# Performance work log

Hardware: AMD Instinct MI355X
Metric: run time of the kernel (lower is better)

Reference implementation:

```python
import jax, jax.numpy as jnp
import numpy as np

B, T, C = 16, 512, 1024
D, K, W = 4096, 128, 8


def _scatter_topk(a, k, use_values):
    """Top-k along last axis; return dense array with top-k values (or 1.0) scattered, zeros elsewhere."""
    shp = a.shape
    a2 = a.reshape(-1, shp[-1])
    vals, idx = jax.lax.top_k(a2, k)
    rows = jnp.arange(a2.shape[0])[:, None]
    src = vals if use_values else jnp.ones_like(vals)
    return jnp.zeros_like(a2).at[rows, idx].set(src).reshape(shp)


def _window_topk(x, k, window_size):
    # x: (B, T, D)
    b, t, d = x.shape
    stride = max(1, window_size // 2)
    if stride >= t:
        num_windows, pad, t_pad = 1, 0, t
    else:
        num_windows = (t - window_size) // stride + 1
        required = (num_windows - 1) * stride + window_size
        pad = max(0, required - t)
        t_pad = t + pad
    if pad > 0:
        x = jnp.pad(x, ((0, 0), (0, pad), (0, 0)))
    starts = jnp.arange(num_windows) * stride                      # (NW,)
    tidx = starts[:, None] + jnp.arange(window_size)               # (NW, W)
    x_windows = x[:, tidx, :]                                      # (B, NW, W, D)
    window_sums = x_windows.sum(axis=2)                            # (B, NW, D)
    mask_windows = _scatter_topk(window_sums, k, use_values=False)  # (B, NW, D)
    votes = (x_windows * mask_windows[:, :, None, :]).reshape(b, num_windows * window_size, d)
    feature_votes = jnp.zeros((b, t_pad, d), x.dtype).at[:, tidx.reshape(-1)].add(votes)
    mask_combined = _scatter_topk(feature_votes, k, use_values=False)  # (B, Tp, D)
    x_sparse = x * mask_combined
    return x_sparse[:, :t - 0, :] if pad > 0 else x_sparse


def setup_inputs() -> dict:
    key = jax.random.key(0)
    ks = jax.random.split(key, 4)
    x_ssl = jax.random.normal(ks[0], (B, T, C), jnp.float32)
    W_dec = jax.random.normal(ks[1], (C, D), jnp.float32)
    W_dec = W_dec / jnp.linalg.norm(W_dec, axis=0, keepdims=True)
    W_enc = W_dec.T                                                # tied init, as in module
    W1 = jax.random.normal(ks[2], (256, D), jnp.float32) * (1.0 / np.sqrt(D))
    W2 = jax.random.normal(ks[3], (2, 256), jnp.float32) * (1.0 / np.sqrt(256))
    return dict(
        x_ssl=x_ssl, W_enc=W_enc, b_enc=jnp.zeros((D,), jnp.float32),
        W_dec=W_dec, b_dec=jnp.zeros((C,), jnp.float32),
        ln_g=jnp.ones((D,), jnp.float32), ln_b=jnp.zeros((D,), jnp.float32),
        W1=W1, b1=jnp.zeros((256,), jnp.float32),
        W2=W2, b2=jnp.zeros((2,), jnp.float32),
    )


def reference(x_ssl, W_enc, b_enc, W_dec, b_dec, ln_g, ln_b, W1, b1, W2, b2):
    b, t, c = x_ssl.shape
    x_flat = x_ssl.reshape(b * t, c)
    # SAE encode with window top-k (window_size=8 > 1 path)
    pre = jnp.einsum('nc,dc->nd', x_flat - b_dec, W_enc) + b_enc
    post_relu = jax.nn.relu(pre).reshape(b, t, -1)                 # (B, T, D)
    encoded = _window_topk(post_relu, K, W)                        # (B, T, D)
    encoded_flat = encoded.reshape(b * t, -1)
    # SAE decode + reconstruction loss
    x_recon = jnp.einsum('nd,cd->nc', encoded_flat, W_dec) + b_dec
    sae_loss = jnp.mean((x_recon - x_flat) ** 2)
    # classifier on pooled sparse features (dropout is inference no-op)
    pooled = encoded.mean(axis=1)                                  # (B, D) == AdaptiveAvgPool1d(1)
    mu = pooled.mean(axis=-1, keepdims=True)
    var = pooled.var(axis=-1, keepdims=True)
    ln = (pooled - mu) / jnp.sqrt(var + 1e-5) * ln_g + ln_b
    h = jax.nn.relu(ln @ W1.T + b1)
    logits = h @ W2.T + b2
    log_probs = jax.nn.log_softmax(logits, axis=-1)
    return log_probs, sae_loss
```

## Files before the change

### kernel.cpp

```cpp
#include <hip/hip_runtime.h>

#define BB   16
#define TT   512
#define CC   1024
#define DD   4096
#define NN   (BB*TT)
#define NWIN 127
#define KTOP 128

typedef __attribute__((ext_vector_type(8))) short short8;
typedef _Float16 half8 __attribute__((ext_vector_type(8)));
typedef __attribute__((ext_vector_type(4))) float f32x4;

__device__ __forceinline__ unsigned short f2bf(float f) {
    unsigned u = __float_as_uint(f);
    unsigned r = (u + 0x7fffu + ((u >> 16) & 1u)) >> 16;
    return (unsigned short)r;
}
__device__ __forceinline__ float bf2f(unsigned x) {
    return __uint_as_float((x & 0xffffu) << 16);
}
__device__ __forceinline__ unsigned short f2h(float f) {
    union { _Float16 h; unsigned short u; } c;
    c.h = (_Float16)f;
    return c.u;
}
__device__ __forceinline__ unsigned tokey(float f) {
    unsigned u = __float_as_uint(f);
    return (u & 0x80000000u) ? ~u : (u | 0x80000000u);
}
__device__ __forceinline__ void async_lds16(const void* g, void* l) {
    __builtin_amdgcn_global_load_lds((const __attribute__((address_space(1))) void*)g,
                                     (__attribute__((address_space(3))) void*)l, 16, 0, 0);
}

__device__ __forceinline__ unsigned wave_prefix_incl(unsigned v) {
    int lane = threadIdx.x & 63;
#pragma unroll
    for (int off = 1; off < 64; off <<= 1) {
        unsigned n = __shfl_up(v, off, 64);
        if (lane >= off) v += n;
    }
    return v;
}
__device__ __forceinline__ unsigned wave_suffix_incl(unsigned v) {
    int lane = threadIdx.x & 63;
#pragma unroll
    for (int off = 1; off < 64; off <<= 1) {
        unsigned n = __shfl_down(v, off, 64);
        if (lane + off < 64) v += n;
    }
    return v;
}

__device__ __forceinline__ unsigned select_top128(const unsigned* keys,
                                                  unsigned* hist, unsigned* shx) {
    const int tid = threadIdx.x, wid = tid >> 6, lane = tid & 63;
    const unsigned ZKEY = 0x80000000u;
    unsigned cpos = 0, cz = 0;
#pragma unroll
    for (int i = 0; i < 16; ++i) {
        cpos += (keys[i] > ZKEY);
        cz   += (keys[i] == ZKEY);
    }
    unsigned ppos = wave_prefix_incl(cpos);
    unsigned pz   = wave_prefix_incl(cz);
    if (lane == 63) { shx[wid] = ppos; shx[4 + wid] = pz; }
    __syncthreads();
    unsigned nz = shx[0] + shx[1] + shx[2] + shx[3];
    unsigned selbits = 0u;
    if (nz <= KTOP) {
        unsigned need = KTOP - nz;
        unsigned zr = pz - cz;
        if (wid > 0) zr += shx[4];
        if (wid > 1) zr += shx[5];
        if (wid > 2) zr += shx[6];
#pragma unroll
        for (int i = 0; i < 16; ++i) {
            bool sel = (keys[i] > ZKEY) || (keys[i] == ZKEY && zr < need);
            if (keys[i] == ZKEY) ++zr;
            selbits |= (sel ? 1u : 0u) << i;
        }
        return selbits;
    }
    unsigned k2[16];
#pragma unroll
    for (int i = 0; i < 16; ++i) k2[i] = (keys[i] > ZKEY) ? keys[i] : 0u;
    unsigned prefix = 0u, pmask = 0u, Kr = KTOP;
    for (int shift = 24; shift >= 0; shift -= 8) {
        hist[tid] = 0u; hist[256 + tid] = 0u; hist[512 + tid] = 0u; hist[768 + tid] = 0u;
        __syncthreads();
        unsigned* h = hist + (wid << 8);
#pragma unroll
        for (int i = 0; i < 16; ++i)
            if (k2[i] && (k2[i] & pmask) == prefix) atomicAdd(&h[(k2[i] >> shift) & 255u], 1u);
        __syncthreads();
        unsigned v = hist[tid] + hist[256 + tid] + hist[512 + tid] + hist[768 + tid];
        unsigned s = wave_suffix_incl(v);
        if (lane == 0) shx[wid] = s;
        __syncthreads();
        unsigned stot = s;
        if (wid == 0) stot += shx[1] + shx[2] + shx[3];
        else if (wid == 1) stot += shx[2] + shx[3];
        else if (wid == 2) stot += shx[3];
        unsigned above = stot - v;
        if (stot >= Kr && above < Kr) { shx[8] = (unsigned)tid; shx[9] = Kr - above; }
        __syncthreads();
        prefix |= shx[8] << shift;
        pmask |= 0xFFu << shift;
        Kr = shx[9];
    }
    unsigned T = prefix, need = Kr;
    unsigned ce = 0;
#pragma unroll
    for (int i = 0; i < 16; ++i) ce += (k2[i] == T);
    unsigned pe = wave_prefix_incl(ce);
    __syncthreads();
    if (lane == 63) shx[4 + wid] = pe;
    __syncthreads();
    unsigned er = pe - ce;
    if (wid > 0) er += shx[4];
    if (wid > 1) er += shx[5];
    if (wid > 2) er += shx[6];
#pragma unroll
    for (int i = 0; i < 16; ++i) {
        bool sel = (k2[i] > T) || (k2[i] == T && er < need);
        if (k2[i] == T) ++er;
        selbits |= (sel ? 1u : 0u) << i;
    }
    return selbits;
}

__global__ __launch_bounds__(256) void k_convert_all(const float* __restrict__ x,
                                                     const float* __restrict__ Wenc,
                                                     const float* __restrict__ Wdec,
                                                     const float* __restrict__ bdec,
                                                     unsigned short* __restrict__ xh,
                                                     unsigned short* __restrict__ wh,
                                                     unsigned short* __restrict__ wdb,
                                                     float* __restrict__ pooled_zero) {
    const int bid = blockIdx.x;
    if (bid < 8192) {
        size_t i = (size_t)bid * 256 + threadIdx.x;
        float4 v = ((const float4*)x)[i];
        size_t c = (i * 4) & (CC - 1);
        v.x -= bdec[c]; v.y -= bdec[c + 1]; v.z -= bdec[c + 2]; v.w -= bdec[c + 3];
        uint2 o;
        o.x = (unsigned)f2h(v.x) | ((unsigned)f2h(v.y) << 16);
        o.y = (unsigned)f2h(v.z) | ((unsigned)f2h(v.w) << 16);
        ((uint2*)xh)[i] = o;
    } else if (bid < 12288) {
        size_t i = (size_t)(bid - 8192) * 256 + threadIdx.x;
        float4 v = ((const float4*)Wenc)[i];
        uint2 o;
        o.x = (unsigned)f2h(v.x) | ((unsigned)f2h(v.y) << 16);
        o.y = (unsigned)f2h(v.z) | ((unsigned)f2h(v.w) << 16);
        ((uint2*)wh)[i] = o;
    } else if (bid < 16384) {
        size_t i = (size_t)(bid - 12288) * 256 + threadIdx.x;
        float4 v = ((const float4*)Wdec)[i];
        uint2 o;
        o.x = (unsigned)f2bf(v.x) | ((unsigned)f2bf(v.y) << 16);
        o.y = (unsigned)f2bf(v.z) | ((unsigned)f2bf(v.w) << 16);
        ((uint2*)wdb)[i] = o;
    } else {
        const int n4 = (BB * DD + 64) / 4;
        for (int i = threadIdx.x; i < n4; i += 256)
            ((float4*)pooled_zero)[i] = make_float4(0.f, 0.f, 0.f, 0.f);
    }
}

__device__ __forceinline__ void stage_tile_swz(const unsigned short* gbase, size_t ldk,
                                               unsigned short* lds, int wave, int lane) {
    const int sub = lane >> 3;
    const int cj  = (lane & 7) ^ sub;
#pragma unroll
    for (int i = 0; i < 4; ++i) {
        int n = wave * 4 + i;
        int r = n * 8 + sub;
        async_lds16(gbase + (size_t)r * ldk + cj * 8, lds + n * 512);
    }
}

__global__ __launch_bounds__(256) void k_gemm_enc_f16(const unsigned short* __restrict__ Ah,
                                                      const unsigned short* __restrict__ Bh,
                                                      const float* __restrict__ bias,
                                                      float* __restrict__ Cout,
                                                      float* __restrict__ gsum,
                                                      int Ndim, int Kdim) {
    __shared__ __align__(16) unsigned short smem[2 * 128 * 64];
    unsigned short* At = smem;
    unsigned short* Bt = smem + 128 * 64;
    float* cbuf = (float*)smem;
    const int tid = threadIdx.x, wave = tid >> 6, lane = tid & 63;
    const int bm = blockIdx.y * 128, bn = blockIdx.x * 128;
    const int wm = (wave >> 1) * 64, wn = (wave & 1) * 64;
    const int rA = lane & 15, q8 = (lane >> 4) * 8, rp7 = rA & 7;
    const int q = lane >> 4, qr = q * 4, cl = lane & 15;
    f32x4 acc[4][4] = {};
    for (int k0 = 0; k0 < Kdim; k0 += 64) {
        __syncthreads();
        stage_tile_swz(Ah + (size_t)bm * Kdim + k0, Kdim, At, wave, lane);
        stage_tile_swz(Bh + (size_t)bn * Kdim + k0, Kdim, Bt, wave, lane);
        __syncthreads();
#pragma unroll
        for (int kk = 0; kk < 64; kk += 32) {
            const int sc = ((((kk + q8) >> 3) ^ rp7) << 3);
            half8 a[4], b[4];
#pragma unroll
            for (int mt = 0; mt < 4; ++mt) a[mt] = *(const half8*)(At + (wm + mt * 16 + rA) * 64 + sc);
#pragma unroll
            for (int nt = 0; nt < 4; ++nt) b[nt] = *(const half8*)(Bt + (wn + nt * 16 + rA) * 64 + sc);
#pragma unroll
            for (int mt = 0; mt < 4; ++mt)
#pragma unroll
                for (int nt = 0; nt < 4; ++nt)
                    acc[mt][nt] = __builtin_amdgcn_mfma_f32_16x16x32_f16(a[mt], b[nt], acc[mt][nt], 0, 0, 0);
        }
    }
    float bv[4];
#pragma unroll
    for (int nt = 0; nt < 4; ++nt) bv[nt] = bias[bn + wn + nt * 16 + cl];
#pragma unroll
    for (int p = 0; p < 2; ++p) {
        __syncthreads();
        if ((wave >> 1) == p) {
#pragma unroll
            for (int nt = 0; nt < 4; ++nt) {
                int lc = wn + nt * 16 + cl;
                int pcb = (lc >> 2) ^ (q << 1);
#pragma unroll
                for (int mt = 0; mt < 4; ++mt) {
#pragma unroll
                    for (int r = 0; r < 4; ++r) {
                        int lr = mt * 16 + qr + r;
                        float v = acc[mt][nt][r] + bv[nt];
                        v = v > 0.f ? v : 0.f;
                        cbuf[lr * 128 + pcb * 4 + (lc & 3)] = v;
                    }
                }
            }
        }
        __syncthreads();
#pragma unroll
        for (int i = 0; i < 2; ++i) {
            int gidx = i * 256 + tid;
            int grow = gidx >> 5;
            int colg = gidx & 31;
            float4 s = make_float4(0.f, 0.f, 0.f, 0.f);
#pragma unroll
            for (int j = 0; j < 4; ++j) {
                int lr = grow * 4 + j;
                int pcr = colg ^ (((lr >> 2) & 3) << 1);
                float4 v = *(const float4*)&cbuf[lr * 128 + pcr * 4];
                s.x += v.x; s.y += v.y; s.z += v.z; s.w += v.w;
                *(float4*)&Cout[(size_t)(bm + p * 64 + lr) * Ndim + bn + colg * 4] = v;
            }
            if (gsum)
                *(float4*)&gsum[(size_t)((bm >> 2) + p * 16 + grow) * Ndim + bn + colg * 4] = s;
        }
    }
}

__global__ __launch_bounds__(256) void k_gemm_recon(const unsigned short* __restrict__ A,
                                                    size_t lda,
                                                    const unsigned short* __restrict__ Bm,
                                                    const float* __restrict__ bdec,
                                                    const float* __restrict__ X,
                                                    float* __restrict__ sae,
                                                    int Ndim, int Kdim) {
    __shared__ __align__(16) unsigned short At[2][128 * 64];
    __shared__ __align__(16) unsigned short Bt[2][128 * 64];
    __shared__ float red[256];
    const int tid = threadIdx.x, wave = tid >> 6, lane = tid & 63;
    const int bm = blockIdx.y * 128, bn = blockIdx.x * 128;
    const int wm = (wave >> 1) * 64, wn = (wave & 1) * 64;
    const int rA = lane & 15, q8 = (lane >> 4) * 8, rp7 = rA & 7;
    f32x4 acc[4][4] = {};
    stage_tile_swz(A + (size_t)bm * lda, lda, At[0], wave, lane);
    stage_tile_swz(Bm + (size_t)bn * Kdim, Kdim, Bt[0], wave, lane);
    __syncthreads();
    for (int k0 = 0; k0 < Kdim; k0 += 64) {
        const int cur = (k0 >> 6) & 1;
        if (k0 + 64 < Kdim) {
            stage_tile_swz(A + (size_t)bm * lda + k0 + 64, lda, At[cur ^ 1], wave, lane);
            stage_tile_swz(Bm + (size_t)bn * Kdim + k0 + 64, Kdim, Bt[cur ^ 1], wave, lane);
        }
#pragma unroll
        for (int kk = 0; kk < 64; kk += 32) {
            const int sc = ((((kk + q8) >> 3) ^ rp7) << 3);
            short8 a[4], b[4];
#pragma unroll
            for (int mt = 0; mt < 4; ++mt) a[mt] = *(const short8*)(At[cur] + (wm + mt * 16 + rA) * 64 + sc);
#pragma unroll
            for (int nt = 0; nt < 4; ++nt) b[nt] = *(const short8*)(Bt[cur] + (wn + nt * 16 + rA) * 64 + sc);
#pragma unroll
            for (int mt = 0; mt < 4; ++mt)
#pragma unroll
                for (int nt = 0; nt < 4; ++nt)
                    acc[mt][nt] = __builtin_amdgcn_mfma_f32_16x16x32_bf16(a[mt], b[nt], acc[mt][nt], 0, 0, 0);
        }
        __syncthreads();
    }
    const int cl = lane & 15, qr = (lane >> 4) * 4;
    float lsum = 0.f;
#pragma unroll
    for (int nt = 0; nt < 4; ++nt) {
        int col = bn + wn + nt * 16 + cl;
        float bv = bdec[col];
#pragma unroll
        for (int mt = 0; mt < 4; ++mt) {
            int row0 = bm + wm + mt * 16 + qr;
#pragma unroll
            for (int r = 0; r < 4; ++r) {
                float v = acc[mt][nt][r] + bv - X[(size_t)(row0 + r) * Ndim + col];
                lsum += v * v;
            }
        }
    }
    red[tid] = lsum;
    __syncthreads();
    for (int s = 128; s > 0; s >>= 1) { if (tid < s) red[tid] += red[tid + s]; __syncthreads(); }
    if (tid == 0) atomicAdd(sae, red[0]);
}

__global__ __launch_bounds__(256) void k_winsum_g(const float* __restrict__ gsum,
                                                  unsigned* __restrict__ wmask) {
    __shared__ unsigned hist[1024];
    __shared__ unsigned shx[16];
    __shared__ unsigned short halves[256];
    const int tid = threadIdx.x, w = blockIdx.x, b = blockIdx.y;
    const float* g0 = gsum + ((size_t)(b * 128 + w)) * DD + tid * 16;
    const float* g1 = g0 + DD;
    unsigned keys[16];
#pragma unroll
    for (int q = 0; q < 4; ++q) {
        float4 u = *(const float4*)(g0 + q * 4);
        float4 v = *(const float4*)(g1 + q * 4);
        keys[q * 4 + 0] = tokey(u.x + v.x);
        keys[q * 4 + 1] = tokey(u.y + v.y);
        keys[q * 4 + 2] = tokey(u.z + v.z);
        keys[q * 4 + 3] = tokey(u.w + v.w);
    }
    unsigned selbits = select_top128(keys, hist, shx);
    halves[tid] = (unsigned short)selbits;
    __syncthreads();
    if (tid < 128)
        wmask[(size_t)(b * NWIN + w) * 128 + tid] =
            (unsigned)halves[2 * tid] | ((unsigned)halves[2 * tid + 1] << 16);
}

__global__ __launch_bounds__(256) void k_winsum_p(const float* __restrict__ post,
                                                  unsigned* __restrict__ wmask) {
    __shared__ unsigned hist[1024];
    __shared__ unsigned shx[16];
    __shared__ unsigned short halves[256];
    const int tid = threadIdx.x, w = blockIdx.x, b = blockIdx.y;
    const float* base = post + (size_t)(b * TT + w * 4) * DD + tid * 16;
    float s[16] = {};
#pragma unroll
    for (int j = 0; j < 8; ++j) {
        const float* rp = base + (size_t)j * DD;
#pragma unroll
        for (int q = 0; q < 4; ++q) {
            float4 u = *(const float4*)(rp + q * 4);
            s[q * 4 + 0] += u.x; s[q * 4 + 1] += u.y; s[q * 4 + 2] += u.z; s[q * 4 + 3] += u.w;
        }
    }
    unsigned keys[16];
#pragma unroll
    for (int i = 0; i < 16; ++i) keys[i] = tokey(s[i]);
    unsigned selbits = select_top128(keys, hist, shx);
    halves[tid] = (unsigned short)selbits;
    __syncthreads();
    if (tid < 128)
        wmask[(size_t)(b * NWIN + w) * 128 + tid] =
            (unsigned)halves[2 * tid] | ((unsigned)halves[2 * tid + 1] << 16);
}

__global__ __launch_bounds__(256) void k_votes(float* __restrict__ post,
                                               const unsigned* __restrict__ wmask,
                                               float* __restrict__ pooled) {
    __shared__ unsigned long long cand[256];
    __shared__ unsigned char selbyte[DD];
    __shared__ unsigned shx[16];
    const int tid = threadIdx.x, wid = tid >> 6, lane = tid & 63;
    const int t = blockIdx.x, b = blockIdx.y;
    float* rp = post + (size_t)(b * TT + t) * DD;
    int w1 = t >> 2, w0 = w1 - 1;
    unsigned mw0 = 0u, mw1 = 0u;
    if (w0 >= 0)        mw0 = wmask[(size_t)(b * NWIN + w0) * 128 + (tid >> 1)];
    if (w1 <= NWIN - 1) mw1 = wmask[(size_t)(b * NWIN + w1) * 128 + (tid >> 1)];
    const int bbase = (tid & 1) * 16;
    const unsigned ZKEY = 0x80000000u;
    float vals[16];
    unsigned keys[16];
#pragma unroll
    for (int q = 0; q < 4; ++q) {
        float4 u = *(const float4*)(rp + tid * 16 + q * 4);
        vals[q * 4 + 0] = u.x; vals[q * 4 + 1] = u.y; vals[q * 4 + 2] = u.z; vals[q * 4 + 3] = u.w;
    }
#pragma unroll
    for (int i = 0; i < 16; ++i) {
        float cov = (float)(((mw0 >> (bbase + i)) & 1u) + ((mw1 >> (bbase + i)) & 1u));
        keys[i] = tokey(vals[i] * cov);
    }
    unsigned cpos = 0, cz = 0;
#pragma unroll
    for (int i = 0; i < 16; ++i) {
        cpos += (keys[i] > ZKEY);
        cz   += (keys[i] == ZKEY);
    }
    unsigned ppos = wave_prefix_incl(cpos);
    unsigned pz   = wave_prefix_incl(cz);
    if (lane == 63) { shx[wid] = ppos; shx[4 + wid] = pz; }
    __syncthreads();
    unsigned nz = shx[0] + shx[1] + shx[2] + shx[3];
    unsigned selbits = 0u;
    if (nz <= KTOP) {
        unsigned need = KTOP - nz;
        unsigned zr = pz - cz;
        if (wid > 0) zr += shx[4];
        if (wid > 1) zr += shx[5];
        if (wid > 2) zr += shx[6];
#pragma unroll
        for (int i = 0; i < 16; ++i) {
            bool sel = (keys[i] > ZKEY) || (keys[i] == ZKEY && zr < need);
            if (keys[i] == ZKEY) ++zr;
            selbits |= (sel ? 1u : 0u) << i;
        }
    } else {
        *(uint4*)(selbyte + tid * 16) = make_uint4(0u, 0u, 0u, 0u);
        unsigned off = ppos - cpos;
        if (wid > 0) off += shx[0];
        if (wid > 1) off += shx[1];
        if (wid > 2) off += shx[2];
#pragma unroll
        for (int i = 0; i < 16; ++i) {
            if (keys[i] > ZKEY && off < 256u) {
                int d = tid * 16 + i;
                cand[off++] = ((unsigned long long)keys[i] << 12) | (unsigned)(4095 - d);
            }
        }
        __syncthreads();
        unsigned m = nz < 256u ? nz : 256u;
        if ((unsigned)tid < m) {
            unsigned long long mine = cand[tid];
            unsigned rank = 0;
            for (unsigned j = 0; j < m; ++j) rank += (cand[j] > mine);
            if (rank < KTOP) selbyte[4095 - (unsigned)(mine & 0xFFFu)] = 1;
        }
        __syncthreads();
#pragma unroll
        for (int i = 0; i < 16; ++i)
            selbits |= (selbyte[tid * 16 + i] ? 1u : 0u) << i;
    }
    unsigned packed[8];
#pragma unroll
    for (int i = 0; i < 16; i += 2) {
        float v0 = (selbits >> i) & 1u ? vals[i] : 0.f;
        float v1 = (selbits >> (i + 1)) & 1u ? vals[i + 1] : 0.f;
        if (v0 != 0.f) atomicAdd(&pooled[(size_t)b * DD + tid * 16 + i], v0);
        if (v1 != 0.f) atomicAdd(&pooled[(size_t)b * DD + tid * 16 + i + 1], v1);
        packed[i >> 1] = (unsigned)f2bf(v0) | ((unsigned)f2bf(v1) << 16);
    }
    unsigned short* op = (unsigned short*)rp;
    *(uint4*)(op + tid * 16)     = *(uint4*)&packed[0];
    *(uint4*)(op + tid * 16 + 8) = *(uint4*)&packed[4];
}

__device__ __forceinline__ float block_sum(float v, float* red) {
    const int tid = threadIdx.x;
    red[tid] = v;
    __syncthreads();
    for (int s = 128; s > 0; s >>= 1) { if (tid < s) red[tid] += red[tid + s]; __syncthreads(); }
    float r = red[0];
    __syncthreads();
    return r;
}

__global__ __launch_bounds__(256) void k_head_ln(const float* __restrict__ pooled,
                                                 const float* __restrict__ lng,
                                                 const float* __restrict__ lnb,
                                                 float* __restrict__ lnout) {
    __shared__ float red[256];
    const int b = blockIdx.x, tid = threadIdx.x;
    float pv[16];
    float s = 0.f;
#pragma unroll
    for (int q = 0; q < 4; ++q) {
        float4 u = *(const float4*)(pooled + (size_t)b * DD + tid * 16 + q * 4);
        pv[q * 4 + 0] = u.x * (1.f / TT); pv[q * 4 + 1] = u.y * (1.f / TT);
        pv[q * 4 + 2] = u.z * (1.f / TT); pv[q * 4 + 3] = u.w * (1.f / TT);
        s += pv[q * 4 + 0] + pv[q * 4 + 1] + pv[q * 4 + 2] + pv[q * 4 + 3];
    }
    float mean = block_sum(s, red) * (1.f / (float)DD);
    float vs = 0.f;
#pragma unroll
    for (int i = 0; i < 16; ++i) { float c = pv[i] - mean; vs += c * c; }
    float var = block_sum(vs, red) * (1.f / (float)DD);
    float inv = rsqrtf(var + 1e-5f);
#pragma unroll
    for (int q = 0; q < 4; ++q) {
        float4 g = *(const float4*)(lng + tid * 16 + q * 4);
        float4 bb = *(const float4*)(lnb + tid * 16 + q * 4);
        float4 o;
        o.x = (pv[q * 4 + 0] - mean) * inv * g.x + bb.x;
        o.y = (pv[q * 4 + 1] - mean) * inv * g.y + bb.y;
        o.z = (pv[q * 4 + 2] - mean) * inv * g.z + bb.z;
        o.w = (pv[q * 4 + 3] - mean) * inv * g.w + bb.w;
        *(float4*)(lnout + (size_t)b * DD + tid * 16 + q * 4) = o;
    }
}

__global__ __launch_bounds__(256) void k_head_mlp(const float* __restrict__ lnout,
                                                  const float* __restrict__ W1,
                                                  const float* __restrict__ b1,
                                                  float* __restrict__ h) {
    const int gw = (blockIdx.x * 256 + threadIdx.x) >> 6;
    const int lane = threadIdx.x & 63;
    const int b = gw >> 8, row = gw & 255;
    const float* lp = lnout + (size_t)b * DD;
    const float* wr = W1 + (size_t)row * DD;
    float a = 0.f;
#pragma unroll
    for (int k = 0; k < DD / 64; ++k)
        a += lp[lane + 64 * k] * wr[lane + 64 * k];
#pragma unroll
    for (int off = 32; off > 0; off >>= 1) a += __shfl_down(a, off, 64);
    if (lane == 0) h[b * 256 + row] = fmaxf(a + b1[row], 0.f);
}

__global__ __launch_bounds__(256) void k_head_out(const float* __restrict__ h,
                                                  const float* __restrict__ W2,
                                                  const float* __restrict__ b2,
                                                  const float* __restrict__ sae,
                                                  float* __restrict__ out) {
    __shared__ float red[256];
    const int b = blockIdx.x, tid = threadIdx.x;
    float hv = h[b * 256 + tid];
    float l0 = block_sum(hv * W2[tid], red) + b2[0];
    float l1 = block_sum(hv * W2[256 + tid], red) + b2[1];
    if (tid == 0) {
        float m = fmaxf(l0, l1);
        float lse = m + logf(expf(l0 - m) + expf(l1 - m));
        out[2 * b] = l0 - lse;
        out[2 * b + 1] = l1 - lse;
        if (b == 0) out[32] = sae[0] * (1.f / (float)((size_t)NN * CC));
    }
}

extern "C" void kernel_launch(void* const* d_in, const int* in_sizes, int n_in,
                              void* d_out, int out_size, void* d_ws, size_t ws_size,
                              hipStream_t stream) {
    const float* x    = (const float*)d_in[0];
    const float* Wenc = (const float*)d_in[1];
    const float* benc = (const float*)d_in[2];
    const float* Wdec = (const float*)d_in[3];
    const float* bdec = (const float*)d_in[4];
    const float* lng  = (const float*)d_in[5];
    const float* lnb  = (const float*)d_in[6];
    const float* W1   = (const float*)d_in[7];
    const float* b1   = (const float*)d_in[8];
    const float* W2   = (const float*)d_in[9];
    const float* b2   = (const float*)d_in[10];
    float* out = (float*)d_out;

    char* ws = (char*)d_ws;
    float*          post  = (float*)(ws + 0);
    unsigned short* xh16  = (unsigned short*)(ws + 134217728);
    unsigned short* scr   = (unsigned short*)(ws + 150994944);
    unsigned short* wh16  = (unsigned short*)(ws + 167772160);
    unsigned short* wdecb = (unsigned short*)(ws + 184549376);
    unsigned*       wmask = (unsigned*)(ws + 192937984);
    float*          pooled= (float*)(ws + 193978368);
    float*          sae   = (float*)(ws + 194240512);
    float*          gsum  = (float*)(ws + 194240768);
    const bool use_gsum = ws_size >= (size_t)194240768 + 33554432;
    float* gptr = use_gsum ? gsum : nullptr;
    float* lnout = (float*)xh16;
    float* hbuf  = (float*)scr;

    k_convert_all<<<dim3(16385), 256, 0, stream>>>(x, Wenc, Wdec, bdec, xh16, wh16, wdecb, pooled);

    k_gemm_enc_f16<<<dim3(DD / 128, NN / 128), 256, 0, stream>>>(xh16, wh16, benc, post, gptr, DD, CC);
    if (use_gsum)
        k_winsum_g<<<dim3(NWIN, BB), 256, 0, stream>>>(gsum, wmask);
    else
        k_winsum_p<<<dim3(NWIN, BB), 256, 0, stream>>>(post, wmask);
    k_votes<<<dim3(TT, BB), 256, 0, stream>>>(post, wmask, pooled);
    k_gemm_recon<<<dim3(CC / 128, NN / 128), 256, 0, stream>>>((const unsigned short*)post, (size_t)2 * DD,
                                                               wdecb, bdec, x, sae, CC, DD);
    k_head_ln<<<dim3(BB), 256, 0, stream>>>(pooled, lng, lnb, lnout);
    k_head_mlp<<<dim3(1024), 256, 0, stream>>>(lnout, W1, b1, hbuf);
    k_head_out<<<dim3(BB), 256, 0, stream>>>(hbuf, W2, b2, sae, out);
}
```

Before: 450.4 us.

## Store post-ReLU activations in fp16 and use f16 MFMA for decode GEMM

The encoder GEMM now writes its output as fp16 instead of fp32, halving the traffic for the large post-activation buffer. The window-sum, vote and reconstruction kernels are adapted to read fp16, and the votes kernel writes the masked fp16 values back in place. The decoder weights move from bf16 to fp16 so the reconstruction GEMM uses f16 MFMA. Both GEMMs also gain a block-index remap that spreads neighbouring workgroups across 8 groups, likely to improve cache locality across XCDs. fp16 rounding of the activations can change top-k tie-breaking and selection compared with fp32.

```diff
diff --git a/kernel.cpp b/kernel.cpp
--- a/kernel.cpp
+++ b/kernel.cpp
@@ -9,6 +9,7 @@
 #define KTOP 128
 
 typedef __attribute__((ext_vector_type(8))) short short8;
+typedef __attribute__((ext_vector_type(8))) unsigned short ushort8;
 typedef _Float16 half8 __attribute__((ext_vector_type(8)));
 typedef __attribute__((ext_vector_type(4))) float f32x4;
 
@@ -17,13 +18,15 @@
     unsigned r = (u + 0x7fffu + ((u >> 16) & 1u)) >> 16;
     return (unsigned short)r;
 }
-__device__ __forceinline__ float bf2f(unsigned x) {
-    return __uint_as_float((x & 0xffffu) << 16);
-}
 __device__ __forceinline__ unsigned short f2h(float f) {
     union { _Float16 h; unsigned short u; } c;
     c.h = (_Float16)f;
     return c.u;
+}
+__device__ __forceinline__ float h2f(unsigned short u) {
+    union { unsigned short u; _Float16 h; } c;
+    c.u = u;
+    return (float)c.h;
 }
 __device__ __forceinline__ unsigned tokey(float f) {
     unsigned u = __float_as_uint(f);
@@ -137,7 +140,7 @@
                                                      const float* __restrict__ bdec,
                                                      unsigned short* __restrict__ xh,
                                                      unsigned short* __restrict__ wh,
-                                                     unsigned short* __restrict__ wdb,
+                                                     unsigned short* __restrict__ wdh,
                                                      float* __restrict__ pooled_zero) {
     const int bid = blockIdx.x;
     if (bid < 8192) {
@@ -160,9 +163,9 @@
         size_t i = (size_t)(bid - 12288) * 256 + threadIdx.x;
         float4 v = ((const float4*)Wdec)[i];
         uint2 o;
-        o.x = (unsigned)f2bf(v.x) | ((unsigned)f2bf(v.y) << 16);
-        o.y = (unsigned)f2bf(v.z) | ((unsigned)f2bf(v.w) << 16);
-        ((uint2*)wdb)[i] = o;
+        o.x = (unsigned)f2h(v.x) | ((unsigned)f2h(v.y) << 16);
+        o.y = (unsigned)f2h(v.z) | ((unsigned)f2h(v.w) << 16);
+        ((uint2*)wdh)[i] = o;
     } else {
         const int n4 = (BB * DD + 64) / 4;
         for (int i = threadIdx.x; i < n4; i += 256)
@@ -185,7 +188,7 @@
 __global__ __launch_bounds__(256) void k_gemm_enc_f16(const unsigned short* __restrict__ Ah,
                                                       const unsigned short* __restrict__ Bh,
                                                       const float* __restrict__ bias,
-                                                      float* __restrict__ Cout,
+                                                      unsigned short* __restrict__ Cout,
                                                       float* __restrict__ gsum,
                                                       int Ndim, int Kdim) {
     __shared__ __align__(16) unsigned short smem[2 * 128 * 64];
@@ -193,7 +196,11 @@
     unsigned short* Bt = smem + 128 * 64;
     float* cbuf = (float*)smem;
     const int tid = threadIdx.x, wave = tid >> 6, lane = tid & 63;
-    const int bm = blockIdx.y * 128, bn = blockIdx.x * 128;
+    unsigned nwg  = gridDim.x * gridDim.y;
+    unsigned wid0 = blockIdx.y * gridDim.x + blockIdx.x;
+    unsigned widx = (wid0 & 7u) * (nwg >> 3) + (wid0 >> 3);
+    const int bn = (int)(widx % gridDim.x) * 128;
+    const int bm = (int)(widx / gridDim.x) * 128;
     const int wm = (wave >> 1) * 64, wn = (wave & 1) * 64;
     const int rA = lane & 15, q8 = (lane >> 4) * 8, rp7 = rA & 7;
     const int q = lane >> 4, qr = q * 4, cl = lane & 15;
@@ -254,7 +261,10 @@
                 int pcr = colg ^ (((lr >> 2) & 3) << 1);
                 float4 v = *(const float4*)&cbuf[lr * 128 + pcr * 4];
                 s.x += v.x; s.y += v.y; s.z += v.z; s.w += v.w;
-                *(float4*)&Cout[(size_t)(bm + p * 64 + lr) * Ndim + bn + colg * 4] = v;
+                uint2 o;
+                o.x = (unsigned)f2h(v.x) | ((unsigned)f2h(v.y) << 16);
+                o.y = (unsigned)f2h(v.z) | ((unsigned)f2h(v.w) << 16);
+                *(uint2*)&Cout[(size_t)(bm + p * 64 + lr) * Ndim + bn + colg * 4] = o;
             }
             if (gsum)
                 *(float4*)&gsum[(size_t)((bm >> 2) + p * 16 + grow) * Ndim + bn + colg * 4] = s;
@@ -273,7 +283,11 @@
     __shared__ __align__(16) unsigned short Bt[2][128 * 64];
     __shared__ float red[256];
     const int tid = threadIdx.x, wave = tid >> 6, lane = tid & 63;
-    const int bm = blockIdx.y * 128, bn = blockIdx.x * 128;
+    unsigned nwg  = gridDim.x * gridDim.y;
+    unsigned wid0 = blockIdx.y * gridDim.x + blockIdx.x;
+    unsigned widx = (wid0 & 7u) * (nwg >> 3) + (wid0 >> 3);
+    const int bn = (int)(widx % gridDim.x) * 128;
+    const int bm = (int)(widx / gridDim.x) * 128;
     const int wm = (wave >> 1) * 64, wn = (wave & 1) * 64;
     const int rA = lane & 15, q8 = (lane >> 4) * 8, rp7 = rA & 7;
     f32x4 acc[4][4] = {};
@@ -289,16 +303,16 @@
 #pragma unroll
         for (int kk = 0; kk < 64; kk += 32) {
             const int sc = ((((kk + q8) >> 3) ^ rp7) << 3);
-            short8 a[4], b[4];
-#pragma unroll
-            for (int mt = 0; mt < 4; ++mt) a[mt] = *(const short8*)(At[cur] + (wm + mt * 16 + rA) * 64 + sc);
-#pragma unroll
-            for (int nt = 0; nt < 4; ++nt) b[nt] = *(const short8*)(Bt[cur] + (wn + nt * 16 + rA) * 64 + sc);
+            half8 a[4], b[4];
+#pragma unroll
+            for (int mt = 0; mt < 4; ++mt) a[mt] = *(const half8*)(At[cur] + (wm + mt * 16 + rA) * 64 + sc);
+#pragma unroll
+            for (int nt = 0; nt < 4; ++nt) b[nt] = *(const half8*)(Bt[cur] + (wn + nt * 16 + rA) * 64 + sc);
 #pragma unroll
             for (int mt = 0; mt < 4; ++mt)
 #pragma unroll
                 for (int nt = 0; nt < 4; ++nt)
-                    acc[mt][nt] = __builtin_amdgcn_mfma_f32_16x16x32_bf16(a[mt], b[nt], acc[mt][nt], 0, 0, 0);
+                    acc[mt][nt] = __builtin_amdgcn_mfma_f32_16x16x32_f16(a[mt], b[nt], acc[mt][nt], 0, 0, 0);
         }
         __syncthreads();
     }
@@ -350,22 +364,21 @@
             (unsigned)halves[2 * tid] | ((unsigned)halves[2 * tid + 1] << 16);
 }
 
-__global__ __launch_bounds__(256) void k_winsum_p(const float* __restrict__ post,
+__global__ __launch_bounds__(256) void k_winsum_p(const unsigned short* __restrict__ post,
                                                   unsigned* __restrict__ wmask) {
     __shared__ unsigned hist[1024];
     __shared__ unsigned shx[16];
     __shared__ unsigned short halves[256];
     const int tid = threadIdx.x, w = blockIdx.x, b = blockIdx.y;
-    const float* base = post + (size_t)(b * TT + w * 4) * DD + tid * 16;
+    const unsigned short* base = post + (size_t)(b * TT + w * 4) * DD + tid * 16;
     float s[16] = {};
 #pragma unroll
     for (int j = 0; j < 8; ++j) {
-        const float* rp = base + (size_t)j * DD;
-#pragma unroll
-        for (int q = 0; q < 4; ++q) {
-            float4 u = *(const float4*)(rp + q * 4);
-            s[q * 4 + 0] += u.x; s[q * 4 + 1] += u.y; s[q * 4 + 2] += u.z; s[q * 4 + 3] += u.w;
-        }
+        const unsigned short* rp = base + (size_t)j * DD;
+        ushort8 u0 = *(const ushort8*)rp;
+        ushort8 u1 = *(const ushort8*)(rp + 8);
+#pragma unroll
+        for (int i = 0; i < 8; ++i) { s[i] += h2f(u0[i]); s[8 + i] += h2f(u1[i]); }
     }
     unsigned keys[16];
 #pragma unroll
@@ -378,7 +391,7 @@
             (unsigned)halves[2 * tid] | ((unsigned)halves[2 * tid + 1] << 16);
 }
 
-__global__ __launch_bounds__(256) void k_votes(float* __restrict__ post,
+__global__ __launch_bounds__(256) void k_votes(unsigned short* __restrict__ post,
                                                const unsigned* __restrict__ wmask,
                                                float* __restrict__ pooled) {
     __shared__ unsigned long long cand[256];
@@ -386,20 +399,19 @@
     __shared__ unsigned shx[16];
     const int tid = threadIdx.x, wid = tid >> 6, lane = tid & 63;
     const int t = blockIdx.x, b = blockIdx.y;
-    float* rp = post + (size_t)(b * TT + t) * DD;
+    unsigned short* rp = post + (size_t)(b * TT + t) * DD;
     int w1 = t >> 2, w0 = w1 - 1;
     unsigned mw0 = 0u, mw1 = 0u;
     if (w0 >= 0)        mw0 = wmask[(size_t)(b * NWIN + w0) * 128 + (tid >> 1)];
     if (w1 <= NWIN - 1) mw1 = wmask[(size_t)(b * NWIN + w1) * 128 + (tid >> 1)];
     const int bbase = (tid & 1) * 16;
     const unsigned ZKEY = 0x80000000u;
+    ushort8 raw0 = *(const ushort8*)(rp + tid * 16);
+    ushort8 raw1 = *(const ushort8*)(rp + tid * 16 + 8);
     float vals[16];
+#pragma unroll
+    for (int i = 0; i < 8; ++i) { vals[i] = h2f(raw0[i]); vals[8 + i] = h2f(raw1[i]); }
     unsigned keys[16];
-#pragma unroll
-    for (int q = 0; q < 4; ++q) {
-        float4 u = *(const float4*)(rp + tid * 16 + q * 4);
-        vals[q * 4 + 0] = u.x; vals[q * 4 + 1] = u.y; vals[q * 4 + 2] = u.z; vals[q * 4 + 3] = u.w;
-    }
 #pragma unroll
     for (int i = 0; i < 16; ++i) {
         float cov = (float)(((mw0 >> (bbase + i)) & 1u) + ((mw1 >> (bbase + i)) & 1u));
@@ -455,18 +467,18 @@
         for (int i = 0; i < 16; ++i)
             selbits |= (selbyte[tid * 16 + i] ? 1u : 0u) << i;
     }
-    unsigned packed[8];
-#pragma unroll
-    for (int i = 0; i < 16; i += 2) {
-        float v0 = (selbits >> i) & 1u ? vals[i] : 0.f;
-        float v1 = (selbits >> (i + 1)) & 1u ? vals[i + 1] : 0.f;
-        if (v0 != 0.f) atomicAdd(&pooled[(size_t)b * DD + tid * 16 + i], v0);
-        if (v1 != 0.f) atomicAdd(&pooled[(size_t)b * DD + tid * 16 + i + 1], v1);
-        packed[i >> 1] = (unsigned)f2bf(v0) | ((unsigned)f2bf(v1) << 16);
-    }
-    unsigned short* op = (unsigned short*)rp;
-    *(uint4*)(op + tid * 16)     = *(uint4*)&packed[0];
-    *(uint4*)(op + tid * 16 + 8) = *(uint4*)&packed[4];
+    ushort8 o0, o1;
+#pragma unroll
+    for (int i = 0; i < 8; ++i) {
+        bool s0 = (selbits >> i) & 1u;
+        bool s1 = (selbits >> (8 + i)) & 1u;
+        o0[i] = s0 ? raw0[i] : (unsigned short)0;
+        o1[i] = s1 ? raw1[i] : (unsigned short)0;
+        if (s0 && vals[i] != 0.f)     atomicAdd(&pooled[(size_t)b * DD + tid * 16 + i], vals[i]);
+        if (s1 && vals[8 + i] != 0.f) atomicAdd(&pooled[(size_t)b * DD + tid * 16 + 8 + i], vals[8 + i]);
+    }
+    *(ushort8*)(rp + tid * 16)     = o0;
+    *(ushort8*)(rp + tid * 16 + 8) = o1;
 }
 
 __device__ __forceinline__ float block_sum(float v, float* red) {
@@ -567,21 +579,21 @@
     float* out = (float*)d_out;
 
     char* ws = (char*)d_ws;
-    float*          post  = (float*)(ws + 0);
-    unsigned short* xh16  = (unsigned short*)(ws + 134217728);
-    unsigned short* scr   = (unsigned short*)(ws + 150994944);
-    unsigned short* wh16  = (unsigned short*)(ws + 167772160);
-    unsigned short* wdecb = (unsigned short*)(ws + 184549376);
-    unsigned*       wmask = (unsigned*)(ws + 192937984);
-    float*          pooled= (float*)(ws + 193978368);
-    float*          sae   = (float*)(ws + 194240512);
-    float*          gsum  = (float*)(ws + 194240768);
-    const bool use_gsum = ws_size >= (size_t)194240768 + 33554432;
+    unsigned short* post  = (unsigned short*)(ws + 0);
+    unsigned short* xh16  = (unsigned short*)(ws + 67108864);
+    unsigned short* scr   = (unsigned short*)(ws + 83886080);
+    unsigned short* wh16  = (unsigned short*)(ws + 100663296);
+    unsigned short* wd16  = (unsigned short*)(ws + 109051904);
+    unsigned*       wmask = (unsigned*)(ws + 117440512);
+    float*          pooled= (float*)(ws + 118480896);
+    float*          sae   = (float*)(ws + 118743040);
+    float*          gsum  = (float*)(ws + 118743296);
+    const bool use_gsum = ws_size >= (size_t)118743296 + 33554432;
     float* gptr = use_gsum ? gsum : nullptr;
     float* lnout = (float*)xh16;
     float* hbuf  = (float*)scr;
 
-    k_convert_all<<<dim3(16385), 256, 0, stream>>>(x, Wenc, Wdec, bdec, xh16, wh16, wdecb, pooled);
+    k_convert_all<<<dim3(16385), 256, 0, stream>>>(x, Wenc, Wdec, bdec, xh16, wh16, wd16, pooled);
 
     k_gemm_enc_f16<<<dim3(DD / 128, NN / 128), 256, 0, stream>>>(xh16, wh16, benc, post, gptr, DD, CC);
     if (use_gsum)
@@ -589,8 +601,8 @@
     else
         k_winsum_p<<<dim3(NWIN, BB), 256, 0, stream>>>(post, wmask);
     k_votes<<<dim3(TT, BB), 256, 0, stream>>>(post, wmask, pooled);
-    k_gemm_recon<<<dim3(CC / 128, NN / 128), 256, 0, stream>>>((const unsigned short*)post, (size_t)2 * DD,
-                                                               wdecb, bdec, x, sae, CC, DD);
+    k_gemm_recon<<<dim3(CC / 128, NN / 128), 256, 0, stream>>>(post, (size_t)DD,
+                                                               wd16, bdec, x, sae, CC, DD);
     k_head_ln<<<dim3(BB), 256, 0, stream>>>(pooled, lng, lnb, lnout);
     k_head_mlp<<<dim3(1024), 256, 0, stream>>>(lnout, W1, b1, hbuf);
     k_head_out<<<dim3(BB), 256, 0, stream>>>(hbuf, W2, b2, sae, out);
```

Result: no change. 442.2 us (-1.8%).
